# Performance work log

Measured on AMD Instinct MI355X. Metric: run time of the kernel, lower is better.

Reference implementation:

```python
import jax, jax.numpy as jnp
import numpy as np

B, S, I, H = 512, 1024, 20, 64  # batch, seq_len, input_size, hidden_size


def setup_inputs() -> dict:
    key = jax.random.key(0)
    ks = jax.random.split(key, 12)
    # one-hot protein sequences with variable true lengths (padding is all-zero rows)
    lengths = jax.random.randint(ks[0], (B,), 100, S + 1)
    tokens = jax.random.randint(ks[1], (B, S), 0, I)
    valid = (jnp.arange(S)[None, :] < lengths[:, None]).astype(jnp.float32)
    input1 = jax.nn.one_hot(tokens, I, dtype=jnp.float32) * valid[:, :, None]

    def nrm(k, shape, s=0.05):
        return jax.random.normal(k, shape, jnp.float32) * s

    return {
        'input1': input1,
        'W_ih_f': nrm(ks[2], (4 * H, I)), 'W_hh_f': nrm(ks[3], (4 * H, H)), 'b_f': nrm(ks[4], (4 * H,)),
        'W_ih_b': nrm(ks[5], (4 * H, I)), 'W_hh_b': nrm(ks[6], (4 * H, H)), 'b_b': nrm(ks[7], (4 * H,)),
        'conv1_w': nrm(ks[8], (20, 20), 1.0),           # blosum pssm: [out_c=20, kernel_w=20]
        'conv2_w': nrm(ks[9], (100, 4, 20)), 'conv2_b': nrm(ks[9], (100,)),
        'fc1_w': nrm(ks[10], (64, 228)), 'fc1_b': nrm(ks[10], (64,)),
        'fc2_w': nrm(ks[11], (2, 64)), 'fc2_b': nrm(ks[11], (2,)),
    }


def _lstm_final(x, W_ih, W_hh, b):
    # x: [B,S,I] -> final hidden state [B,H]; torch gate order i,f,g,o
    xs = jnp.einsum('bsi,gi->sbg', x, W_ih) + b  # [S,B,4H]

    def step(carry, gx):
        h, c = carry
        g = gx + h @ W_hh.T
        i, f, gg, o = jnp.split(g, 4, axis=-1)
        c = jax.nn.sigmoid(f) * c + jax.nn.sigmoid(i) * jnp.tanh(gg)
        h = jax.nn.sigmoid(o) * jnp.tanh(c)
        return (h, c), None

    init = (jnp.zeros((x.shape[0], H), x.dtype), jnp.zeros((x.shape[0], H), x.dtype))
    (h, _), _ = jax.lax.scan(step, init, xs)
    return h


def reference(input1, W_ih_f, W_hh_f, b_f, W_ih_b, W_hh_b, b_b,
              conv1_w, conv2_w, conv2_b, fc1_w, fc1_b, fc2_w, fc2_b):
    # BiLSTM: final hidden state of each direction (dropout is identity in eval)
    h_fw = _lstm_final(input1, W_ih_f, W_hh_f, b_f)
    h_bw = _lstm_final(input1[:, ::-1, :], W_ih_b, W_hh_b, b_b)
    lstm_output = jnp.concatenate([h_fw, h_bw], axis=1)  # [B,128]

    # conv1: kernel (1,20) spans the full width -> per-position linear map. [B,20,S]
    c1 = jnp.einsum('bsj,cj->bcs', input1, conv1_w)
    # faithful torch.reshape (B,20,S,1)->(B,S,1,20): row-major reinterpretation
    c1 = c1.reshape(input1.shape[0], S, 20)  # [B,S,20]

    # ragged 4-bin segment mean over the first width[i]=4*(len[i]//4) positions
    lens = jnp.sum(input1, axis=(1, 2)).astype(jnp.int32)
    bw = jnp.floor(lens / 4).astype(jnp.int32)
    width = bw * 4
    pos = jnp.arange(S)[None, :]                       # [1,S]
    bin_idx = pos // bw[:, None]                       # [B,S]
    valid = pos < width[:, None]                       # [B,S]
    mask = ((bin_idx[:, None, :] == jnp.arange(4)[None, :, None]) & valid[:, None, :]).astype(c1.dtype)  # [B,4,S]
    avblock = jnp.einsum('bks,bsc->bkc', mask, c1) / bw.astype(c1.dtype)[:, None, None]  # [B,4,20]

    # conv2: kernel (4,20) spans the whole avblock -> one dot per out channel
    c2 = jnp.einsum('bkc,okc->bo', avblock, conv2_w) + conv2_b  # [B,100]
    c2 = jax.nn.relu(c2)

    merged = jnp.concatenate([lstm_output, c2], axis=1)  # [B,228]
    fc1 = merged @ fc1_w.T + fc1_b
    fc2 = fc1 @ fc2_w.T + fc2_b
    return jax.nn.softmax(fc2, axis=1)
```

## Files before the change

### kernel.cpp

```cpp
#include <hip/hip_runtime.h>
#include <hip/hip_bf16.h>

#define BB 512
#define SS 1024
#define NI 20
#define HH 64
#define NG 256
#define MB4 4
#define PAD 72
#define TSTR 257

typedef unsigned short u16;
typedef unsigned int u32;
typedef unsigned long long u64;
typedef _Float16 f16;
typedef f16 f16x8 __attribute__((ext_vector_type(8)));
typedef float f32x4 __attribute__((ext_vector_type(4)));

#define LOG2E 1.4426950408889634f

__device__ __forceinline__ float bf2f(u16 b) { return __uint_as_float(((u32)b) << 16); }
__device__ __forceinline__ float ldw(const void* p, int idx, int mode) {
  return mode ? bf2f(((const u16*)p)[idx]) : ((const float*)p)[idx];
}
__device__ __forceinline__ float frcp(float x) { return __builtin_amdgcn_rcpf(x); }
__device__ __forceinline__ float fexp2(float x) { return __builtin_amdgcn_exp2f(x); }

__global__ __launch_bounds__(256)
void lstm_kernel(const void* in1,
                 const void* Wih_f, const void* Whh_f, const void* b_f,
                 const void* Wih_b, const void* Whh_b, const void* b_b,
                 short* toks_g, int* lens, float* hout) {
  int bx = blockIdx.x;
  int dir = bx >> 7;
  int b0 = (bx & 127) * MB4;
  int t = threadIdx.x;
  int w = t >> 6, lane = t & 63, l = lane & 15, q = lane >> 4;
  int bsel = l >> 2;

  __shared__ __align__(16) float table[21 * TSTR];
  __shared__ __align__(16) f16 hbuf[2][MB4][PAD];
  __shared__ short tok_s[SS * MB4];
  __shared__ u64 red[256];
  __shared__ int mode_sh;

  if (t == 0) mode_sh = 1;
  __syncthreads();
  {
    float v = bf2f(((const u16*)b_f)[t]);
    if (!(fabsf(v) < 1000.0f)) atomicAnd(&mode_sh, 0);
  }
  __syncthreads();
  int mode = mode_sh;
  const void* Wih = dir ? Wih_b : Wih_f;
  const void* Whh = dir ? Whh_b : Whh_f;
  const void* bv  = dir ? b_b   : b_f;

  u64 cnt = 0;
  for (int m = 0; m < MB4; ++m) {
    if (mode) {
      u32* st = (u32*)table;
      for (int k0 = 0; k0 < 4; ++k0) {
        const u32* src = (const u32*)in1 + ((size_t)(b0 + m) * SS + k0 * 256) * 10;
#pragma unroll
        for (int i = 0; i < 10; ++i) st[t + i * 256] = src[t + i * 256];
        __syncthreads();
        const u32* row = st + t * 10;
        int tok = -1;
#pragma unroll
        for (int ww = 0; ww < 10; ++ww) {
          u32 u = row[ww];
          if (u & 0xFFFFu) tok = 2 * ww;
          if (u >> 16)     tok = 2 * ww + 1;
        }
        tok_s[(k0 * 256 + t) * MB4 + m] = (short)(tok + 1);
        if (dir == 0) toks_g[(size_t)(b0 + m) * SS + k0 * 256 + t] = (short)tok;
        cnt += (u64)(tok >= 0) << (16 * m);
        __syncthreads();
      }
    } else {
      float4* st = (float4*)table;
      for (int k0 = 0; k0 < 4; ++k0) {
        const float4* src = (const float4*)((const float*)in1 + ((size_t)(b0 + m) * SS + k0 * 256) * 20);
#pragma unroll
        for (int i = 0; i < 5; ++i) st[t + i * 256] = src[t + i * 256];
        __syncthreads();
        const float* row = (const float*)table + t * 20;
        int tok = -1;
#pragma unroll
        for (int ww = 0; ww < 20; ++ww)
          if (row[ww] != 0.f) tok = ww;
        tok_s[(k0 * 256 + t) * MB4 + m] = (short)(tok + 1);
        if (dir == 0) toks_g[(size_t)(b0 + m) * SS + k0 * 256 + t] = (short)tok;
        cnt += (u64)(tok >= 0) << (16 * m);
        __syncthreads();
      }
    }
  }
  red[t] = cnt;
  __syncthreads();
  for (int stp = 128; stp > 0; stp >>= 1) {
    if (t < stp) red[t] += red[t + stp];
    __syncthreads();
  }
  if (dir == 0 && t < MB4)
    lens[b0 + t] = (int)((red[0] >> (16 * t)) & 0xFFFFull);
  __syncthreads();

  for (int idx = t; idx < 21 * 256; idx += 256) {
    int r = idx >> 8, g = idx & 255;
    float scl = ((g >> 6) == 2) ? (2.f * LOG2E) : (-LOG2E);
    float v = ldw(bv, g, mode);
    if (r > 0) v += ldw(Wih, g * NI + (r - 1), mode);
    table[r * TSTR + g] = scl * v;
  }
  f16x8 Bf[4][2];
#pragma unroll
  for (int tt = 0; tt < 4; ++tt) {
    float scl = (tt == 2) ? (2.f * LOG2E) : (-LOG2E);
    int g = 64 * tt + 16 * w + l;
#pragma unroll
    for (int kc = 0; kc < 2; ++kc) {
      f16x8 v;
#pragma unroll
      for (int j = 0; j < 8; ++j)
        v[j] = (f16)(scl * ldw(Whh, g * HH + kc * 32 + q * 8 + j, mode));
      Bf[tt][kc] = v;
    }
  }
  for (int idx = t; idx < 2 * MB4 * PAD; idx += 256)
    ((f16*)hbuf)[idx] = (f16)0.f;
  __syncthreads();

  float c_st = 0.f, hlast = 0.f;
  int jj = 16 * w + l;
  int tbase = 16 * w + l;

  float wxc[4];
  {
    int pos0 = dir ? (SS - 1) : 0;
    int base = (int)tok_s[pos0 * MB4 + q] * TSTR + tbase;
    wxc[0] = table[base];       wxc[1] = table[base + 64];
    wxc[2] = table[base + 128]; wxc[3] = table[base + 192];
  }
  int tok1;
  {
    int pos1 = dir ? (SS - 2) : 1;
    tok1 = (int)tok_s[pos1 * MB4 + q];
  }

#pragma unroll 2
  for (int s = 0; s < SS; ++s) {
    int p = s & 1;
    f16x8 a0 = *(const f16x8*)&hbuf[p][bsel][q * 8];
    f16x8 a1 = *(const f16x8*)&hbuf[p][bsel][32 + q * 8];
    float wxn[4];
    {
      int base = tok1 * TSTR + tbase;
      wxn[0] = table[base];       wxn[1] = table[base + 64];
      wxn[2] = table[base + 128]; wxn[3] = table[base + 192];
    }
    {
      int pos2 = (dir ? (SS - 3 - s) : (s + 2)) & (SS - 1);
      tok1 = (int)tok_s[pos2 * MB4 + q];
    }

    f32x4 acc[4];
#pragma unroll
    for (int tt = 0; tt < 4; ++tt) {
      f32x4 ci = {wxc[tt], wxc[tt], wxc[tt], wxc[tt]};
      acc[tt] = __builtin_amdgcn_mfma_f32_16x16x32_f16(a0, Bf[tt][0], ci, 0, 0, 0);
    }
#pragma unroll
    for (int tt = 0; tt < 4; ++tt)
      acc[tt] = __builtin_amdgcn_mfma_f32_16x16x32_f16(a1, Bf[tt][1], acc[tt], 0, 0, 0);

    {
      float Ei = fexp2(acc[0][0]);
      float Ef = fexp2(acc[1][0]);
      float G  = fexp2(acc[2][0]);
      float Eo = fexp2(acc[3][0]);
      float Ei1 = Ei + 1.f, Ef1 = Ef + 1.f, G1 = G + 1.f, Gm = G - 1.f;
      float t1 = Ei1 * G1;
      float num = fmaf(c_st, t1, Gm * Ef1);
      float cv = num * frcp(t1 * Ef1);
      c_st = cv;
      float C = fexp2((2.f * LOG2E) * cv);
      float hv = (C - 1.f) * frcp((Eo + 1.f) * (C + 1.f));
      hlast = hv;
      hbuf[p ^ 1][q][jj] = (f16)hv;
    }
    __syncthreads();
    wxc[0] = wxn[0]; wxc[1] = wxn[1]; wxc[2] = wxn[2]; wxc[3] = wxn[3];
  }
  hout[(b0 + q) * 128 + dir * 64 + jj] = hlast;
}

__global__ void head_kernel(const void* conv1_w, const void* conv2_w, const void* conv2_b,
                            const void* fc1_w, const void* fc1_b,
                            const void* fc2_w, const void* fc2_b,
                            const void* bvec, const short* toks, const int* lens,
                            const float* hout, void* out) {
  int b = blockIdx.x;
  int t = threadIdx.x;
  __shared__ float c1w[400];
  __shared__ short tok_s[SS];
  __shared__ float pav[2][80];
  __shared__ float avg[80];
  __shared__ float merged[228];
  __shared__ float fpart[4][64];
  __shared__ float fc1v[64];
  __shared__ int mode_sh;

  if (t == 0) mode_sh = 1;
  __syncthreads();
  {
    float v = bf2f(((const u16*)bvec)[t]);
    if (!(fabsf(v) < 1000.0f)) atomicAnd(&mode_sh, 0);
  }
  __syncthreads();
  int mode = mode_sh;

  for (int i = t; i < 400; i += 256) c1w[i] = ldw(conv1_w, i, mode);
  for (int s = t; s < SS; s += 256) tok_s[s] = toks[(size_t)b * SS + s];
  __syncthreads();

  int len = lens[b];
  int bw = len >> 2;
  if (t < 160) {
    int half = t / 80;
    int u = t - half * 80;
    int k = u / 20, cc = u % 20;
    int start = k * bw, mid = k * bw + (bw >> 1), end = (k + 1) * bw;
    int s0 = half ? mid : start;
    int s1 = half ? end : mid;
    float sum = 0.f;
    for (int s = s0; s < s1; ++s) {
      int f = s * 20 + cc;
      int ch = f >> 10;
      int pos = f & 1023;
      int tk = tok_s[pos];
      if (tk >= 0) sum += c1w[ch * 20 + tk];
    }
    pav[half][u] = sum;
  }
  __syncthreads();
  if (t < 80) avg[t] = (pav[0][t] + pav[1][t]) / (float)bw;
  __syncthreads();

  if (t < 128) merged[t] = hout[b * 128 + t];
  if (t >= 128 && t < 228) {
    int o = t - 128;
    float dot = ldw(conv2_b, o, mode);
#pragma unroll
    for (int q = 0; q < 80; ++q)
      dot += avg[q] * ldw(conv2_w, o * 80 + q, mode);
    merged[t] = dot > 0.f ? dot : 0.f;
  }
  __syncthreads();

  {
    int o = t & 63, ch = t >> 6;
    float v = 0.f;
    int m0 = ch * 57, m1 = m0 + 57;
    for (int m = m0; m < m1; ++m)
      v += merged[m] * ldw(fc1_w, o * 228 + m, mode);
    fpart[ch][o] = v;
  }
  __syncthreads();
  if (t < 64)
    fc1v[t] = fpart[0][t] + fpart[1][t] + fpart[2][t] + fpart[3][t] + ldw(fc1_b, t, mode);
  __syncthreads();

  if (t == 0) {
    float x0 = ldw(fc2_b, 0, mode), x1 = ldw(fc2_b, 1, mode);
    for (int m = 0; m < 64; ++m) {
      x0 += fc1v[m] * ldw(fc2_w, m, mode);
      x1 += fc1v[m] * ldw(fc2_w, 64 + m, mode);
    }
    float mx = fmaxf(x0, x1);
    float e0 = fexp2(LOG2E * (x0 - mx)), e1 = fexp2(LOG2E * (x1 - mx));
    float inv = 1.f / (e0 + e1);
    if (mode) {
      ((__hip_bfloat16*)out)[b * 2 + 0] = __float2bfloat16(e0 * inv);
      ((__hip_bfloat16*)out)[b * 2 + 1] = __float2bfloat16(e1 * inv);
    } else {
      ((float*)out)[b * 2 + 0] = e0 * inv;
      ((float*)out)[b * 2 + 1] = e1 * inv;
    }
  }
}

extern "C" void kernel_launch(void* const* d_in, const int* in_sizes, int n_in,
                              void* d_out, int out_size, void* d_ws, size_t ws_size,
                              hipStream_t stream) {
  (void)in_sizes; (void)n_in; (void)out_size; (void)ws_size;
  char* ws = (char*)d_ws;
  int*   lens = (int*)(ws + 256);
  short* toks = (short*)(ws + 256 + 2048);
  float* hout = (float*)(ws + 256 + 2048 + (size_t)BB * SS * sizeof(short));

  lstm_kernel<<<256, 256, 0, stream>>>(d_in[0],
                                       d_in[1], d_in[2], d_in[3],
                                       d_in[4], d_in[5], d_in[6],
                                       toks, lens, hout);
  head_kernel<<<BB, 256, 0, stream>>>(d_in[7], d_in[8], d_in[9],
                                      d_in[10], d_in[11], d_in[12], d_in[13],
                                      d_in[3], toks, lens, hout, d_out);
}
```

Before: 423.5 us.

## Merge forward and backward LSTM directions into one 512-thread block

The LSTM kernel now runs both directions for a group of four sequences in a single 512-thread block (128 blocks instead of 256), with separate gate tables and hidden buffers per direction. Token extraction and length counting from the input happen once per block instead of twice. The head kernel also stages fc1 weights in shared memory before the dot products. The trade-off is that the two directions now share one barrier per timestep across 8 waves, the block count halves, and LDS use per block grows, which may lower occupancy or lengthen the serial recurrence.

```diff
diff --git a/kernel.cpp b/kernel.cpp
--- a/kernel.cpp
+++ b/kernel.cpp
@@ -26,94 +26,101 @@
 __device__ __forceinline__ float frcp(float x) { return __builtin_amdgcn_rcpf(x); }
 __device__ __forceinline__ float fexp2(float x) { return __builtin_amdgcn_exp2f(x); }
 
-__global__ __launch_bounds__(256)
+__global__ __launch_bounds__(512)
 void lstm_kernel(const void* in1,
                  const void* Wih_f, const void* Whh_f, const void* b_f,
                  const void* Wih_b, const void* Whh_b, const void* b_b,
                  short* toks_g, int* lens, float* hout) {
   int bx = blockIdx.x;
-  int dir = bx >> 7;
-  int b0 = (bx & 127) * MB4;
+  int b0 = bx * MB4;
   int t = threadIdx.x;
-  int w = t >> 6, lane = t & 63, l = lane & 15, q = lane >> 4;
+  int wave = t >> 6;
+  int dir = wave >> 2;
+  int w = wave & 3;
+  int lane = t & 63, l = lane & 15, q = lane >> 4;
   int bsel = l >> 2;
 
-  __shared__ __align__(16) float table[21 * TSTR];
-  __shared__ __align__(16) f16 hbuf[2][MB4][PAD];
+  __shared__ __align__(16) float tabF[21 * TSTR];
+  __shared__ __align__(16) float tabB[21 * TSTR];
+  __shared__ __align__(16) f16 hbuf[2][2][MB4][PAD];
   __shared__ short tok_s[SS * MB4];
   __shared__ u64 red[256];
   __shared__ int mode_sh;
 
   if (t == 0) mode_sh = 1;
   __syncthreads();
-  {
+  if (t < 256) {
     float v = bf2f(((const u16*)b_f)[t]);
     if (!(fabsf(v) < 1000.0f)) atomicAnd(&mode_sh, 0);
   }
   __syncthreads();
   int mode = mode_sh;
-  const void* Wih = dir ? Wih_b : Wih_f;
-  const void* Whh = dir ? Whh_b : Whh_f;
-  const void* bv  = dir ? b_b   : b_f;
 
   u64 cnt = 0;
   for (int m = 0; m < MB4; ++m) {
     if (mode) {
-      u32* st = (u32*)table;
+      u32* st = (u32*)tabF;
       for (int k0 = 0; k0 < 4; ++k0) {
         const u32* src = (const u32*)in1 + ((size_t)(b0 + m) * SS + k0 * 256) * 10;
-#pragma unroll
-        for (int i = 0; i < 10; ++i) st[t + i * 256] = src[t + i * 256];
+        for (int i = t; i < 2560; i += 512) st[i] = src[i];
         __syncthreads();
-        const u32* row = st + t * 10;
-        int tok = -1;
-#pragma unroll
-        for (int ww = 0; ww < 10; ++ww) {
-          u32 u = row[ww];
-          if (u & 0xFFFFu) tok = 2 * ww;
-          if (u >> 16)     tok = 2 * ww + 1;
+        if (t < 256) {
+          const u32* row = st + t * 10;
+          int tok = -1;
+#pragma unroll
+          for (int ww = 0; ww < 10; ++ww) {
+            u32 u = row[ww];
+            if (u & 0xFFFFu) tok = 2 * ww;
+            if (u >> 16)     tok = 2 * ww + 1;
+          }
+          tok_s[(k0 * 256 + t) * MB4 + m] = (short)(tok + 1);
+          toks_g[(size_t)(b0 + m) * SS + k0 * 256 + t] = (short)tok;
+          cnt += (u64)(tok >= 0) << (16 * m);
         }
-        tok_s[(k0 * 256 + t) * MB4 + m] = (short)(tok + 1);
-        if (dir == 0) toks_g[(size_t)(b0 + m) * SS + k0 * 256 + t] = (short)tok;
-        cnt += (u64)(tok >= 0) << (16 * m);
         __syncthreads();
       }
     } else {
-      float4* st = (float4*)table;
+      float4* st = (float4*)tabF;
       for (int k0 = 0; k0 < 4; ++k0) {
         const float4* src = (const float4*)((const float*)in1 + ((size_t)(b0 + m) * SS + k0 * 256) * 20);
-#pragma unroll
-        for (int i = 0; i < 5; ++i) st[t + i * 256] = src[t + i * 256];
+        for (int i = t; i < 1280; i += 512) st[i] = src[i];
         __syncthreads();
-        const float* row = (const float*)table + t * 20;
-        int tok = -1;
-#pragma unroll
-        for (int ww = 0; ww < 20; ++ww)
-          if (row[ww] != 0.f) tok = ww;
-        tok_s[(k0 * 256 + t) * MB4 + m] = (short)(tok + 1);
-        if (dir == 0) toks_g[(size_t)(b0 + m) * SS + k0 * 256 + t] = (short)tok;
-        cnt += (u64)(tok >= 0) << (16 * m);
+        if (t < 256) {
+          const float* row = (const float*)tabF + t * 20;
+          int tok = -1;
+#pragma unroll
+          for (int ww = 0; ww < 20; ++ww)
+            if (row[ww] != 0.f) tok = ww;
+          tok_s[(k0 * 256 + t) * MB4 + m] = (short)(tok + 1);
+          toks_g[(size_t)(b0 + m) * SS + k0 * 256 + t] = (short)tok;
+          cnt += (u64)(tok >= 0) << (16 * m);
+        }
         __syncthreads();
       }
     }
   }
-  red[t] = cnt;
+  if (t < 256) red[t] = cnt;
   __syncthreads();
   for (int stp = 128; stp > 0; stp >>= 1) {
     if (t < stp) red[t] += red[t + stp];
     __syncthreads();
   }
-  if (dir == 0 && t < MB4)
+  if (t < MB4)
     lens[b0 + t] = (int)((red[0] >> (16 * t)) & 0xFFFFull);
   __syncthreads();
 
-  for (int idx = t; idx < 21 * 256; idx += 256) {
-    int r = idx >> 8, g = idx & 255;
+  for (int idx = t; idx < 2 * 21 * 256; idx += 512) {
+    int d2 = idx / 5376;
+    int rem = idx - d2 * 5376;
+    int r = rem >> 8, g = rem & 255;
+    const void* Wih2 = d2 ? Wih_b : Wih_f;
+    const void* bv2  = d2 ? b_b   : b_f;
     float scl = ((g >> 6) == 2) ? (2.f * LOG2E) : (-LOG2E);
-    float v = ldw(bv, g, mode);
-    if (r > 0) v += ldw(Wih, g * NI + (r - 1), mode);
-    table[r * TSTR + g] = scl * v;
-  }
+    float v = ldw(bv2, g, mode);
+    if (r > 0) v += ldw(Wih2, g * NI + (r - 1), mode);
+    (d2 ? tabB : tabF)[r * TSTR + g] = scl * v;
+  }
+  const void* Whh = dir ? Whh_b : Whh_f;
   f16x8 Bf[4][2];
 #pragma unroll
   for (int tt = 0; tt < 4; ++tt) {
@@ -128,10 +135,11 @@
       Bf[tt][kc] = v;
     }
   }
-  for (int idx = t; idx < 2 * MB4 * PAD; idx += 256)
+  for (int idx = t; idx < 2 * 2 * MB4 * PAD; idx += 512)
     ((f16*)hbuf)[idx] = (f16)0.f;
   __syncthreads();
 
+  const float* tab = dir ? tabB : tabF;
   float c_st = 0.f, hlast = 0.f;
   int jj = 16 * w + l;
   int tbase = 16 * w + l;
@@ -140,8 +148,8 @@
   {
     int pos0 = dir ? (SS - 1) : 0;
     int base = (int)tok_s[pos0 * MB4 + q] * TSTR + tbase;
-    wxc[0] = table[base];       wxc[1] = table[base + 64];
-    wxc[2] = table[base + 128]; wxc[3] = table[base + 192];
+    wxc[0] = tab[base];       wxc[1] = tab[base + 64];
+    wxc[2] = tab[base + 128]; wxc[3] = tab[base + 192];
   }
   int tok1;
   {
@@ -152,13 +160,13 @@
 #pragma unroll 2
   for (int s = 0; s < SS; ++s) {
     int p = s & 1;
-    f16x8 a0 = *(const f16x8*)&hbuf[p][bsel][q * 8];
-    f16x8 a1 = *(const f16x8*)&hbuf[p][bsel][32 + q * 8];
+    f16x8 a0 = *(const f16x8*)&hbuf[dir][p][bsel][q * 8];
+    f16x8 a1 = *(const f16x8*)&hbuf[dir][p][bsel][32 + q * 8];
     float wxn[4];
     {
       int base = tok1 * TSTR + tbase;
-      wxn[0] = table[base];       wxn[1] = table[base + 64];
-      wxn[2] = table[base + 128]; wxn[3] = table[base + 192];
+      wxn[0] = tab[base];       wxn[1] = tab[base + 64];
+      wxn[2] = tab[base + 128]; wxn[3] = tab[base + 192];
     }
     {
       int pos2 = (dir ? (SS - 3 - s) : (s + 2)) & (SS - 1);
@@ -188,7 +196,7 @@
       float C = fexp2((2.f * LOG2E) * cv);
       float hv = (C - 1.f) * frcp((Eo + 1.f) * (C + 1.f));
       hlast = hv;
-      hbuf[p ^ 1][q][jj] = (f16)hv;
+      hbuf[dir][p ^ 1][q][jj] = (f16)hv;
     }
     __syncthreads();
     wxc[0] = wxn[0]; wxc[1] = wxn[1]; wxc[2] = wxn[2]; wxc[3] = wxn[3];
@@ -210,6 +218,7 @@
   __shared__ float merged[228];
   __shared__ float fpart[4][64];
   __shared__ float fc1v[64];
+  __shared__ float f1w[64 * 228];
   __shared__ int mode_sh;
 
   if (t == 0) mode_sh = 1;
@@ -222,6 +231,7 @@
   int mode = mode_sh;
 
   for (int i = t; i < 400; i += 256) c1w[i] = ldw(conv1_w, i, mode);
+  for (int i = t; i < 64 * 228; i += 256) f1w[i] = ldw(fc1_w, i, mode);
   for (int s = t; s < SS; s += 256) tok_s[s] = toks[(size_t)b * SS + s];
   __syncthreads();
 
@@ -264,7 +274,7 @@
     float v = 0.f;
     int m0 = ch * 57, m1 = m0 + 57;
     for (int m = m0; m < m1; ++m)
-      v += merged[m] * ldw(fc1_w, o * 228 + m, mode);
+      v += merged[m] * f1w[o * 228 + m];
     fpart[ch][o] = v;
   }
   __syncthreads();
@@ -300,7 +310,7 @@
   short* toks = (short*)(ws + 256 + 2048);
   float* hout = (float*)(ws + 256 + 2048 + (size_t)BB * SS * sizeof(short));
 
-  lstm_kernel<<<256, 256, 0, stream>>>(d_in[0],
+  lstm_kernel<<<128, 512, 0, stream>>>(d_in[0],
                                        d_in[1], d_in[2], d_in[3],
                                        d_in[4], d_in[5], d_in[6],
                                        toks, lens, hout);
```

After: 531.1 us. 25.4% more time.

## Stage head weights in shared memory and process two batch rows per block

Applied to the files above, without the earlier changes.

The head kernel now loads conv2, fc1 and fc2 weights into shared memory once per block and processes two batch rows per block, with half as many blocks launched. fc2 becomes a parallel tree reduction instead of a single-thread loop. The LSTM padding constant PAD also changes from 72 to 80, which may alter LDS bank conflicts in the LSTM kernel. This adds roughly 91KB of shared memory per head block, which lowers occupancy, and it adds serial weight-load time at the start of each block.

```diff
diff --git a/kernel.cpp b/kernel.cpp
--- a/kernel.cpp
+++ b/kernel.cpp
@@ -7,7 +7,7 @@
 #define HH 64
 #define NG 256
 #define MB4 4
-#define PAD 72
+#define PAD 80
 #define TSTR 257
 
 typedef unsigned short u16;
@@ -196,14 +196,17 @@
   hout[(b0 + q) * 128 + dir * 64 + jj] = hlast;
 }
 
-__global__ void head_kernel(const void* conv1_w, const void* conv2_w, const void* conv2_b,
-                            const void* fc1_w, const void* fc1_b,
-                            const void* fc2_w, const void* fc2_b,
-                            const void* bvec, const short* toks, const int* lens,
-                            const float* hout, void* out) {
-  int b = blockIdx.x;
+__global__ __launch_bounds__(256)
+void head_kernel(const void* conv1_w, const void* conv2_w, const void* conv2_b,
+                 const void* fc1_w, const void* fc1_b,
+                 const void* fc2_w, const void* fc2_b,
+                 const void* bvec, const short* toks, const int* lens,
+                 const float* hout, void* out) {
   int t = threadIdx.x;
   __shared__ float c1w[400];
+  __shared__ float c2w[100 * 80];
+  __shared__ float f1w[64 * 228];
+  __shared__ float f2w[128];
   __shared__ short tok_s[SS];
   __shared__ float pav[2][80];
   __shared__ float avg[80];
@@ -222,71 +225,88 @@
   int mode = mode_sh;
 
   for (int i = t; i < 400; i += 256) c1w[i] = ldw(conv1_w, i, mode);
-  for (int s = t; s < SS; s += 256) tok_s[s] = toks[(size_t)b * SS + s];
-  __syncthreads();
-
-  int len = lens[b];
-  int bw = len >> 2;
-  if (t < 160) {
-    int half = t / 80;
-    int u = t - half * 80;
-    int k = u / 20, cc = u % 20;
-    int start = k * bw, mid = k * bw + (bw >> 1), end = (k + 1) * bw;
-    int s0 = half ? mid : start;
-    int s1 = half ? end : mid;
-    float sum = 0.f;
-    for (int s = s0; s < s1; ++s) {
-      int f = s * 20 + cc;
-      int ch = f >> 10;
-      int pos = f & 1023;
-      int tk = tok_s[pos];
-      if (tk >= 0) sum += c1w[ch * 20 + tk];
-    }
-    pav[half][u] = sum;
-  }
-  __syncthreads();
-  if (t < 80) avg[t] = (pav[0][t] + pav[1][t]) / (float)bw;
-  __syncthreads();
-
-  if (t < 128) merged[t] = hout[b * 128 + t];
-  if (t >= 128 && t < 228) {
-    int o = t - 128;
-    float dot = ldw(conv2_b, o, mode);
-#pragma unroll
-    for (int q = 0; q < 80; ++q)
-      dot += avg[q] * ldw(conv2_w, o * 80 + q, mode);
-    merged[t] = dot > 0.f ? dot : 0.f;
-  }
-  __syncthreads();
-
-  {
-    int o = t & 63, ch = t >> 6;
-    float v = 0.f;
-    int m0 = ch * 57, m1 = m0 + 57;
-    for (int m = m0; m < m1; ++m)
-      v += merged[m] * ldw(fc1_w, o * 228 + m, mode);
-    fpart[ch][o] = v;
-  }
-  __syncthreads();
-  if (t < 64)
-    fc1v[t] = fpart[0][t] + fpart[1][t] + fpart[2][t] + fpart[3][t] + ldw(fc1_b, t, mode);
-  __syncthreads();
-
-  if (t == 0) {
-    float x0 = ldw(fc2_b, 0, mode), x1 = ldw(fc2_b, 1, mode);
-    for (int m = 0; m < 64; ++m) {
-      x0 += fc1v[m] * ldw(fc2_w, m, mode);
-      x1 += fc1v[m] * ldw(fc2_w, 64 + m, mode);
-    }
-    float mx = fmaxf(x0, x1);
-    float e0 = fexp2(LOG2E * (x0 - mx)), e1 = fexp2(LOG2E * (x1 - mx));
-    float inv = 1.f / (e0 + e1);
-    if (mode) {
-      ((__hip_bfloat16*)out)[b * 2 + 0] = __float2bfloat16(e0 * inv);
-      ((__hip_bfloat16*)out)[b * 2 + 1] = __float2bfloat16(e1 * inv);
-    } else {
-      ((float*)out)[b * 2 + 0] = e0 * inv;
-      ((float*)out)[b * 2 + 1] = e1 * inv;
+  for (int i = t; i < 100 * 80; i += 256) c2w[i] = ldw(conv2_w, i, mode);
+  for (int i = t; i < 64 * 228; i += 256) f1w[i] = ldw(fc1_w, i, mode);
+  if (t < 128) f2w[t] = ldw(fc2_w, t, mode);
+
+  for (int pb = 0; pb < 2; ++pb) {
+    int b = blockIdx.x * 2 + pb;
+    __syncthreads();
+    for (int s = t; s < SS; s += 256) tok_s[s] = toks[(size_t)b * SS + s];
+    __syncthreads();
+
+    int len = lens[b];
+    int bw = len >> 2;
+    if (t < 160) {
+      int half = t / 80;
+      int u = t - half * 80;
+      int k = u / 20, cc = u % 20;
+      int start = k * bw, mid = k * bw + (bw >> 1), end = (k + 1) * bw;
+      int s0 = half ? mid : start;
+      int s1 = half ? end : mid;
+      float sum = 0.f;
+      for (int s = s0; s < s1; ++s) {
+        int f = s * 20 + cc;
+        int ch = f >> 10;
+        int pos = f & 1023;
+        int tk = tok_s[pos];
+        if (tk >= 0) sum += c1w[ch * 20 + tk];
+      }
+      pav[half][u] = sum;
+    }
+    __syncthreads();
+    if (t < 80) avg[t] = (pav[0][t] + pav[1][t]) / (float)bw;
+    __syncthreads();
+
+    if (t < 128) merged[t] = hout[b * 128 + t];
+    if (t >= 128 && t < 228) {
+      int o = t - 128;
+      float dot = ldw(conv2_b, o, mode);
+#pragma unroll
+      for (int q = 0; q < 80; ++q)
+        dot += avg[q] * c2w[o * 80 + q];
+      merged[t] = dot > 0.f ? dot : 0.f;
+    }
+    __syncthreads();
+
+    {
+      int o = t & 63, ch = t >> 6;
+      float v = 0.f;
+      int m0 = ch * 57, m1 = m0 + 57;
+      for (int m = m0; m < m1; ++m)
+        v += merged[m] * f1w[o * 228 + m];
+      fpart[ch][o] = v;
+    }
+    __syncthreads();
+    if (t < 64)
+      fc1v[t] = fpart[0][t] + fpart[1][t] + fpart[2][t] + fpart[3][t] + ldw(fc1_b, t, mode);
+    __syncthreads();
+
+    if (t < 128) {
+      int o = t >> 6, m = t & 63;
+      fpart[o][m] = fc1v[m] * f2w[o * 64 + m];
+    }
+    __syncthreads();
+    for (int stp = 32; stp > 0; stp >>= 1) {
+      if (t < 128) {
+        int o = t >> 6, m = t & 63;
+        if (m < stp) fpart[o][m] += fpart[o][m + stp];
+      }
+      __syncthreads();
+    }
+    if (t == 0) {
+      float x0 = fpart[0][0] + ldw(fc2_b, 0, mode);
+      float x1 = fpart[1][0] + ldw(fc2_b, 1, mode);
+      float mx = fmaxf(x0, x1);
+      float e0 = fexp2(LOG2E * (x0 - mx)), e1 = fexp2(LOG2E * (x1 - mx));
+      float inv = 1.f / (e0 + e1);
+      if (mode) {
+        ((__hip_bfloat16*)out)[b * 2 + 0] = __float2bfloat16(e0 * inv);
+        ((__hip_bfloat16*)out)[b * 2 + 1] = __float2bfloat16(e1 * inv);
+      } else {
+        ((float*)out)[b * 2 + 0] = e0 * inv;
+        ((float*)out)[b * 2 + 1] = e1 * inv;
+      }
     }
   }
 }
@@ -304,7 +324,7 @@
                                        d_in[1], d_in[2], d_in[3],
                                        d_in[4], d_in[5], d_in[6],
                                        toks, lens, hout);
-  head_kernel<<<BB, 256, 0, stream>>>(d_in[7], d_in[8], d_in[9],
-                                      d_in[10], d_in[11], d_in[12], d_in[13],
-                                      d_in[3], toks, lens, hout, d_out);
+  head_kernel<<<256, 256, 0, stream>>>(d_in[7], d_in[8], d_in[9],
+                                       d_in[10], d_in[11], d_in[12], d_in[13],
+                                       d_in[3], toks, lens, hout, d_out);
 }
```

New measurement: 422.5 us. No clear change (-0.2%).

## Fuse CNN head and fc1 into LSTM kernel, split recurrent MFMA chains

Applied to the files above, without the earlier changes.

The conv/fc1 head moves into the tail of the LSTM kernel. Each direction block accumulates its partial fc1 contribution into a zeroed workspace with atomics, and a tiny final kernel applies fc2 and softmax. This drops the token/length/hidden-state round trip through global memory and the 512-block head launch. The two recurrent MFMAs per gate are now issued independently and summed, shortening the dependent chain on the serial critical path. hbuf padding also changes. The cost is an extra zero kernel, float atomics whose summation order is nondeterministic, and more shared memory per block.

```diff
diff --git a/kernel.cpp b/kernel.cpp
--- a/kernel.cpp
+++ b/kernel.cpp
@@ -7,7 +7,7 @@
 #define HH 64
 #define NG 256
 #define MB4 4
-#define PAD 72
+#define PAD 80
 #define TSTR 257
 
 typedef unsigned short u16;
@@ -26,11 +26,17 @@
 __device__ __forceinline__ float frcp(float x) { return __builtin_amdgcn_rcpf(x); }
 __device__ __forceinline__ float fexp2(float x) { return __builtin_amdgcn_exp2f(x); }
 
+__global__ void zero_kernel(float* p) {
+  p[blockIdx.x * 256 + threadIdx.x] = 0.f;
+}
+
 __global__ __launch_bounds__(256)
 void lstm_kernel(const void* in1,
                  const void* Wih_f, const void* Whh_f, const void* b_f,
                  const void* Wih_b, const void* Whh_b, const void* b_b,
-                 short* toks_g, int* lens, float* hout) {
+                 const void* conv1_w, const void* conv2_w, const void* conv2_b,
+                 const void* fc1_w, const void* fc1_b,
+                 float* fc1acc) {
   int bx = blockIdx.x;
   int dir = bx >> 7;
   int b0 = (bx & 127) * MB4;
@@ -42,6 +48,11 @@
   __shared__ __align__(16) f16 hbuf[2][MB4][PAD];
   __shared__ short tok_s[SS * MB4];
   __shared__ u64 red[256];
+  __shared__ float w1s[64 * 65];
+  __shared__ float hs[MB4][64];
+  __shared__ float c2r[MB4][100];
+  __shared__ float avg2[80];
+  __shared__ float c1w2[400];
   __shared__ int mode_sh;
 
   if (t == 0) mode_sh = 1;
@@ -74,7 +85,6 @@
           if (u >> 16)     tok = 2 * ww + 1;
         }
         tok_s[(k0 * 256 + t) * MB4 + m] = (short)(tok + 1);
-        if (dir == 0) toks_g[(size_t)(b0 + m) * SS + k0 * 256 + t] = (short)tok;
         cnt += (u64)(tok >= 0) << (16 * m);
         __syncthreads();
       }
@@ -91,7 +101,6 @@
         for (int ww = 0; ww < 20; ++ww)
           if (row[ww] != 0.f) tok = ww;
         tok_s[(k0 * 256 + t) * MB4 + m] = (short)(tok + 1);
-        if (dir == 0) toks_g[(size_t)(b0 + m) * SS + k0 * 256 + t] = (short)tok;
         cnt += (u64)(tok >= 0) << (16 * m);
         __syncthreads();
       }
@@ -103,8 +112,12 @@
     if (t < stp) red[t] += red[t + stp];
     __syncthreads();
   }
-  if (dir == 0 && t < MB4)
-    lens[b0 + t] = (int)((red[0] >> (16 * t)) & 0xFFFFull);
+  int len_m[MB4];
+  {
+    u64 r0 = red[0];
+#pragma unroll
+    for (int m = 0; m < MB4; ++m) len_m[m] = (int)((r0 >> (16 * m)) & 0xFFFFull);
+  }
   __syncthreads();
 
   for (int idx = t; idx < 21 * 256; idx += 256) {
@@ -135,6 +148,7 @@
   float c_st = 0.f, hlast = 0.f;
   int jj = 16 * w + l;
   int tbase = 16 * w + l;
+  const f32x4 z4 = {0.f, 0.f, 0.f, 0.f};
 
   float wxc[4];
   {
@@ -165,21 +179,21 @@
       tok1 = (int)tok_s[pos2 * MB4 + q];
     }
 
-    f32x4 acc[4];
+    f32x4 accL[4], accH[4];
 #pragma unroll
     for (int tt = 0; tt < 4; ++tt) {
       f32x4 ci = {wxc[tt], wxc[tt], wxc[tt], wxc[tt]};
-      acc[tt] = __builtin_amdgcn_mfma_f32_16x16x32_f16(a0, Bf[tt][0], ci, 0, 0, 0);
+      accL[tt] = __builtin_amdgcn_mfma_f32_16x16x32_f16(a0, Bf[tt][0], ci, 0, 0, 0);
     }
 #pragma unroll
     for (int tt = 0; tt < 4; ++tt)
-      acc[tt] = __builtin_amdgcn_mfma_f32_16x16x32_f16(a1, Bf[tt][1], acc[tt], 0, 0, 0);
+      accH[tt] = __builtin_amdgcn_mfma_f32_16x16x32_f16(a1, Bf[tt][1], z4, 0, 0, 0);
 
     {
-      float Ei = fexp2(acc[0][0]);
-      float Ef = fexp2(acc[1][0]);
-      float G  = fexp2(acc[2][0]);
-      float Eo = fexp2(acc[3][0]);
+      float Ei = fexp2(accL[0][0] + accH[0][0]);
+      float Ef = fexp2(accL[1][0] + accH[1][0]);
+      float G  = fexp2(accL[2][0] + accH[2][0]);
+      float Eo = fexp2(accL[3][0] + accH[3][0]);
       float Ei1 = Ei + 1.f, Ef1 = Ef + 1.f, G1 = G + 1.f, Gm = G - 1.f;
       float t1 = Ei1 * G1;
       float num = fmaf(c_st, t1, Gm * Ef1);
@@ -193,25 +207,80 @@
     __syncthreads();
     wxc[0] = wxn[0]; wxc[1] = wxn[1]; wxc[2] = wxn[2]; wxc[3] = wxn[3];
   }
-  hout[(b0 + q) * 128 + dir * 64 + jj] = hlast;
-}
-
-__global__ void head_kernel(const void* conv1_w, const void* conv2_w, const void* conv2_b,
-                            const void* fc1_w, const void* fc1_b,
-                            const void* fc2_w, const void* fc2_b,
-                            const void* bvec, const short* toks, const int* lens,
-                            const float* hout, void* out) {
-  int b = blockIdx.x;
+
+  hs[q][jj] = hlast;
+  for (int i = t; i < 64 * 64; i += 256) {
+    int o = i >> 6, u = i & 63;
+    w1s[o * 65 + u] = ldw(fc1_w, o * 228 + dir * 64 + u, mode);
+  }
+  __syncthreads();
+
+  float* fp = (float*)red;
+  for (int m = 0; m < MB4; ++m) {
+    int o = t & 63, g = t >> 6;
+    float v = 0.f;
+#pragma unroll
+    for (int u = g * 16; u < g * 16 + 16; ++u)
+      v = fmaf(w1s[o * 65 + u], hs[m][u], v);
+    fp[g * 64 + o] = v;
+    __syncthreads();
+    if (t < 64)
+      atomicAdd(&fc1acc[(size_t)(b0 + m) * 64 + t],
+                fp[t] + fp[64 + t] + fp[128 + t] + fp[192 + t]);
+    __syncthreads();
+  }
+
+  if (dir == 1) {
+    for (int i = t; i < 400; i += 256) c1w2[i] = ldw(conv1_w, i, mode);
+    __syncthreads();
+    for (int m = 0; m < MB4; ++m) {
+      int bw = len_m[m] >> 2;
+      if (t < 160) {
+        int half = t / 80, u = t - half * 80;
+        int k = u / 20, cc = u % 20;
+        int start = k * bw, mid = start + (bw >> 1), end = start + bw;
+        int s0 = half ? mid : start, s1 = half ? end : mid;
+        float sum = 0.f;
+        for (int s = s0; s < s1; ++s) {
+          int f = s * 20 + cc;
+          int tk = (int)tok_s[(f & 1023) * MB4 + m] - 1;
+          if (tk >= 0) sum += c1w2[(f >> 10) * 20 + tk];
+        }
+        fp[half * 80 + u] = sum;
+      }
+      __syncthreads();
+      if (t < 80) avg2[t] = (fp[t] + fp[80 + t]) / (float)bw;
+      __syncthreads();
+      if (t < 100) {
+        float dot = ldw(conv2_b, t, mode);
+#pragma unroll
+        for (int qq = 0; qq < 80; ++qq)
+          dot += avg2[qq] * ldw(conv2_w, t * 80 + qq, mode);
+        c2r[m][t] = dot > 0.f ? dot : 0.f;
+      }
+      __syncthreads();
+    }
+    for (int m = 0; m < MB4; ++m) {
+      int o = t & 63, g = t >> 6;
+      float v = 0.f;
+#pragma unroll
+      for (int j = g * 25; j < g * 25 + 25; ++j)
+        v = fmaf(ldw(fc1_w, o * 228 + 128 + j, mode), c2r[m][j], v);
+      fp[g * 64 + o] = v;
+      __syncthreads();
+      if (t < 64)
+        atomicAdd(&fc1acc[(size_t)(b0 + m) * 64 + t],
+                  fp[t] + fp[64 + t] + fp[128 + t] + fp[192 + t] + ldw(fc1_b, t, mode));
+      __syncthreads();
+    }
+  }
+}
+
+__global__ void fin_kernel(const float* fc1acc, const void* fc2_w, const void* fc2_b,
+                           const void* bvec, void* out) {
   int t = threadIdx.x;
-  __shared__ float c1w[400];
-  __shared__ short tok_s[SS];
-  __shared__ float pav[2][80];
-  __shared__ float avg[80];
-  __shared__ float merged[228];
-  __shared__ float fpart[4][64];
-  __shared__ float fc1v[64];
   __shared__ int mode_sh;
-
+  __shared__ float f2w[128];
   if (t == 0) mode_sh = 1;
   __syncthreads();
   {
@@ -220,74 +289,27 @@
   }
   __syncthreads();
   int mode = mode_sh;
-
-  for (int i = t; i < 400; i += 256) c1w[i] = ldw(conv1_w, i, mode);
-  for (int s = t; s < SS; s += 256) tok_s[s] = toks[(size_t)b * SS + s];
-  __syncthreads();
-
-  int len = lens[b];
-  int bw = len >> 2;
-  if (t < 160) {
-    int half = t / 80;
-    int u = t - half * 80;
-    int k = u / 20, cc = u % 20;
-    int start = k * bw, mid = k * bw + (bw >> 1), end = (k + 1) * bw;
-    int s0 = half ? mid : start;
-    int s1 = half ? end : mid;
-    float sum = 0.f;
-    for (int s = s0; s < s1; ++s) {
-      int f = s * 20 + cc;
-      int ch = f >> 10;
-      int pos = f & 1023;
-      int tk = tok_s[pos];
-      if (tk >= 0) sum += c1w[ch * 20 + tk];
-    }
-    pav[half][u] = sum;
-  }
-  __syncthreads();
-  if (t < 80) avg[t] = (pav[0][t] + pav[1][t]) / (float)bw;
-  __syncthreads();
-
-  if (t < 128) merged[t] = hout[b * 128 + t];
-  if (t >= 128 && t < 228) {
-    int o = t - 128;
-    float dot = ldw(conv2_b, o, mode);
-#pragma unroll
-    for (int q = 0; q < 80; ++q)
-      dot += avg[q] * ldw(conv2_w, o * 80 + q, mode);
-    merged[t] = dot > 0.f ? dot : 0.f;
-  }
-  __syncthreads();
-
-  {
-    int o = t & 63, ch = t >> 6;
-    float v = 0.f;
-    int m0 = ch * 57, m1 = m0 + 57;
-    for (int m = m0; m < m1; ++m)
-      v += merged[m] * ldw(fc1_w, o * 228 + m, mode);
-    fpart[ch][o] = v;
-  }
-  __syncthreads();
-  if (t < 64)
-    fc1v[t] = fpart[0][t] + fpart[1][t] + fpart[2][t] + fpart[3][t] + ldw(fc1_b, t, mode);
-  __syncthreads();
-
-  if (t == 0) {
-    float x0 = ldw(fc2_b, 0, mode), x1 = ldw(fc2_b, 1, mode);
-    for (int m = 0; m < 64; ++m) {
-      x0 += fc1v[m] * ldw(fc2_w, m, mode);
-      x1 += fc1v[m] * ldw(fc2_w, 64 + m, mode);
-    }
-    float mx = fmaxf(x0, x1);
-    float e0 = fexp2(LOG2E * (x0 - mx)), e1 = fexp2(LOG2E * (x1 - mx));
-    float inv = 1.f / (e0 + e1);
-    if (mode) {
-      ((__hip_bfloat16*)out)[b * 2 + 0] = __float2bfloat16(e0 * inv);
-      ((__hip_bfloat16*)out)[b * 2 + 1] = __float2bfloat16(e1 * inv);
-    } else {
-      ((float*)out)[b * 2 + 0] = e0 * inv;
-      ((float*)out)[b * 2 + 1] = e1 * inv;
-    }
+  if (t < 128) f2w[t] = ldw(fc2_w, t, mode);
+  __syncthreads();
+
+  int b = blockIdx.x * 256 + t;
+  const float* f = fc1acc + (size_t)b * 64;
+  float x0 = ldw(fc2_b, 0, mode), x1 = ldw(fc2_b, 1, mode);
+#pragma unroll
+  for (int m = 0; m < 64; ++m) {
+    float fv = f[m];
+    x0 = fmaf(fv, f2w[m], x0);
+    x1 = fmaf(fv, f2w[64 + m], x1);
+  }
+  float mx = fmaxf(x0, x1);
+  float e0 = fexp2(LOG2E * (x0 - mx)), e1 = fexp2(LOG2E * (x1 - mx));
+  float inv = frcp(e0 + e1);
+  if (mode) {
+    ((__hip_bfloat16*)out)[b * 2 + 0] = __float2bfloat16(e0 * inv);
+    ((__hip_bfloat16*)out)[b * 2 + 1] = __float2bfloat16(e1 * inv);
+  } else {
+    ((float*)out)[b * 2 + 0] = e0 * inv;
+    ((float*)out)[b * 2 + 1] = e1 * inv;
   }
 }
 
@@ -295,16 +317,14 @@
                               void* d_out, int out_size, void* d_ws, size_t ws_size,
                               hipStream_t stream) {
   (void)in_sizes; (void)n_in; (void)out_size; (void)ws_size;
-  char* ws = (char*)d_ws;
-  int*   lens = (int*)(ws + 256);
-  short* toks = (short*)(ws + 256 + 2048);
-  float* hout = (float*)(ws + 256 + 2048 + (size_t)BB * SS * sizeof(short));
-
+  float* fc1acc = (float*)d_ws;
+
+  zero_kernel<<<128, 256, 0, stream>>>(fc1acc);
   lstm_kernel<<<256, 256, 0, stream>>>(d_in[0],
                                        d_in[1], d_in[2], d_in[3],
                                        d_in[4], d_in[5], d_in[6],
-                                       toks, lens, hout);
-  head_kernel<<<BB, 256, 0, stream>>>(d_in[7], d_in[8], d_in[9],
-                                      d_in[10], d_in[11], d_in[12], d_in[13],
-                                      d_in[3], toks, lens, hout, d_out);
-}
+                                       d_in[7], d_in[8], d_in[9],
+                                       d_in[10], d_in[11],
+                                       fc1acc);
+  fin_kernel<<<2, 256, 0, stream>>>(fc1acc, d_in[12], d_in[13], d_in[3], d_out);
+}
```

Measured after the change: 478.3 us. 12.9% more time.
